# Kernel optimization log

Measured on AMD Instinct MI355X. Metric: run time of the kernel, lower is better.

Reference implementation:

```python
import jax, jax.numpy as jnp
import numpy as np

TEMP = 1.0  # temperature

def setup_inputs() -> dict:
    key = jax.random.key(0)
    ks = jax.random.split(key, 16)
    B, Cin, Cout, H, W, K, kk, A = 32, 64, 64, 128, 128, 4, 3, 16
    c_ = Cin + Cout
    r = lambda k, s: jax.random.normal(k, s, dtype=jnp.float32)
    return {
        'x': r(ks[0], (B, Cin, H, W)),
        'fc_w': r(ks[1], (A, Cin)) * 0.1,
        'ch_w': r(ks[2], (Cin, A)) * 0.1,
        'ch_b': jnp.zeros((Cin,), jnp.float32),
        'f_w': r(ks[3], (Cout, A)) * 0.1,
        'f_b': jnp.zeros((Cout,), jnp.float32),
        'sp_w': r(ks[4], (kk * kk, A)) * 0.1,
        'sp_b': jnp.zeros((kk * kk,), jnp.float32),
        'k_w': r(ks[5], (K, A)) * 0.1,
        'k_b': jnp.zeros((K,), jnp.float32),
        'fus_w1': r(ks[6], (c_ // 16, c_)) * 0.1,
        'fus_b1': jnp.zeros((c_ // 16,), jnp.float32),
        'fus_w2': r(ks[7], (c_, c_ // 16)) * 0.1,
        'fus_b2': jnp.zeros((c_,), jnp.float32),
        'weight': r(ks[8], (K, Cout, Cin, kk, kk)) * (1.0 / np.sqrt(Cin * kk * kk)),
    }

def reference(x, fc_w, ch_w, ch_b, f_w, f_b, sp_w, sp_b, k_w, k_b,
              fus_w1, fus_b1, fus_w2, fus_b2, weight):
    B, Cin, H, W = x.shape
    K, Cout, _, kk, _ = weight.shape
    # --- Attention branches (on globally pooled features) ---
    pooled = x.mean(axis=(2, 3))                      # (B, Cin)
    a = jax.nn.relu(pooled @ fc_w.T)                  # (B, A)
    ch_att = jax.nn.sigmoid(a @ ch_w.T + ch_b)        # (B, Cin)
    f_att = jax.nn.sigmoid(a @ f_w.T + f_b)           # (B, Cout)
    sp_att = jax.nn.sigmoid(a @ sp_w.T + sp_b).reshape(B, 1, 1, 1, kk, kk)
    k_att = jax.nn.softmax((a @ k_w.T + k_b) / TEMP, axis=1).reshape(B, K, 1, 1, 1, 1)
    # --- Attention fusion ---
    att = jnp.concatenate([ch_att, f_att], axis=1)    # (B, Cin+Cout)
    att2 = jax.nn.sigmoid(jax.nn.relu(att @ fus_w1.T + fus_b1) @ fus_w2.T + fus_b2)
    s1 = att2[:, :Cin].sum(axis=1)
    s2 = att2[:, Cin:].sum(axis=1)
    score = jax.nn.softmax(jnp.stack([s1, s2], axis=1) / TEMP, axis=1)
    w1 = score[:, 0][:, None, None, None]
    w2 = score[:, 1][:, None, None, None]
    # --- Apply channel attention, aggregate per-sample weights ---
    xm = w1 * x * ch_att[:, :, None, None]
    # (B,K,1,1,kk,kk)*(B,K,1,1,1,1)*(1,K,Cout,Cin,kk,kk) summed over K
    agg_w = (sp_att * k_att * weight[None]).sum(axis=1)  # (B, Cout, Cin, kk, kk)
    # --- Per-sample conv2d (stride 1, padding 1) ---
    def conv_one(xb, wb):
        return jax.lax.conv_general_dilated(
            xb[None], wb, window_strides=(1, 1), padding=[(1, 1), (1, 1)],
            dimension_numbers=('NCHW', 'OIHW', 'NCHW'))[0]
    out = jax.vmap(conv_one)(xm, agg_w)               # (B, Cout, H, W)
    return w2 * out * f_att[:, :, None, None]
```

## Files before the change

kernel.cpp:

```cpp
#include <hip/hip_runtime.h>
#include <math.h>
#include <stdint.h>

typedef short bf16x8 __attribute__((ext_vector_type(8)));
typedef float f32x16 __attribute__((ext_vector_type(16)));
typedef unsigned short ushort_t;

#define WP_PART 0
#define WP_CIN  65536
#define WP_COUT 67584
#define WP_SP9  69632
#define WP_K4   69920
#define WB_WFB  294912
#define WB_XB   2654208

static __device__ __forceinline__ unsigned f2bf(float f) {
  unsigned u = __builtin_bit_cast(unsigned, f);
  return (u + 0x7FFFu + ((u >> 16) & 1u)) >> 16;
}
static __device__ __forceinline__ unsigned pk2(float a, float b) {
  return f2bf(a) | (f2bf(b) << 16);
}

__global__ __launch_bounds__(256) void convert_kernel(const float* __restrict__ x,
                                                      ushort_t* __restrict__ xb,
                                                      float* __restrict__ part) {
  const int b    = blockIdx.x >> 5;
  const int band = blockIdx.x & 31;
  const int r0   = band << 2;
  const int t    = threadIdx.x;
  const int cp   = t & 31;
  const int seg  = t >> 5;

  __shared__ __align__(16) ushort_t tile[128 * 64];
  __shared__ float red[512];

  float sa = 0.f, sb = 0.f;
  const float* xa  = x + ((size_t)(b * 64 + 2 * cp) * 16384);
  const float* xb_ = xa + 16384;

  for (int r = 0; r < 4; ++r) {
    const int gr = r0 + r;
    const int p0 = gr * 128 + seg * 16;
    float4 a0 = *(const float4*)(xa + p0);
    float4 a1 = *(const float4*)(xa + p0 + 4);
    float4 a2 = *(const float4*)(xa + p0 + 8);
    float4 a3 = *(const float4*)(xa + p0 + 12);
    float4 b0 = *(const float4*)(xb_ + p0);
    float4 b1 = *(const float4*)(xb_ + p0 + 4);
    float4 b2 = *(const float4*)(xb_ + p0 + 8);
    float4 b3 = *(const float4*)(xb_ + p0 + 12);
    sa += (a0.x + a0.y + a0.z + a0.w) + (a1.x + a1.y + a1.z + a1.w) +
          (a2.x + a2.y + a2.z + a2.w) + (a3.x + a3.y + a3.z + a3.w);
    sb += (b0.x + b0.y + b0.z + b0.w) + (b1.x + b1.y + b1.z + b1.w) +
          (b2.x + b2.y + b2.z + b2.w) + (b3.x + b3.y + b3.z + b3.w);

    unsigned* tp = (unsigned*)tile;
    const int base = seg * 16 * 32 + cp;
    tp[base +  0 * 32] = pk2(a0.x, b0.x);
    tp[base +  1 * 32] = pk2(a0.y, b0.y);
    tp[base +  2 * 32] = pk2(a0.z, b0.z);
    tp[base +  3 * 32] = pk2(a0.w, b0.w);
    tp[base +  4 * 32] = pk2(a1.x, b1.x);
    tp[base +  5 * 32] = pk2(a1.y, b1.y);
    tp[base +  6 * 32] = pk2(a1.z, b1.z);
    tp[base +  7 * 32] = pk2(a1.w, b1.w);
    tp[base +  8 * 32] = pk2(a2.x, b2.x);
    tp[base +  9 * 32] = pk2(a2.y, b2.y);
    tp[base + 10 * 32] = pk2(a2.z, b2.z);
    tp[base + 11 * 32] = pk2(a2.w, b2.w);
    tp[base + 12 * 32] = pk2(a3.x, b3.x);
    tp[base + 13 * 32] = pk2(a3.y, b3.y);
    tp[base + 14 * 32] = pk2(a3.z, b3.z);
    tp[base + 15 * 32] = pk2(a3.w, b3.w);
    __syncthreads();

    ushort_t* xbr = xb + ((size_t)(b * 16384 + gr * 128)) * 64;
#pragma unroll
    for (int i = 0; i < 4; ++i) {
      const int s = i * 256 + t;
      uint4 v = *(const uint4*)((const char*)tile + s * 16);
      *(uint4*)(xbr + (size_t)s * 8) = v;
    }
    __syncthreads();
  }

  red[t] = sa;
  red[256 + t] = sb;
  __syncthreads();
  if (t < 64) {
    const int ci = t;
    const int base = (ci & 1) * 256 + (ci >> 1);
    float s = 0.f;
#pragma unroll
    for (int k = 0; k < 8; ++k) s += red[base + k * 32];
    part[((size_t)b * 32 + band) * 64 + ci] = s;
  }
}

__global__ __launch_bounds__(128) void att_kernel(
    const float* __restrict__ pin, int n_part,
    const float* __restrict__ fc_w, const float* __restrict__ ch_w, const float* __restrict__ ch_b,
    const float* __restrict__ f_w,  const float* __restrict__ f_b,
    const float* __restrict__ sp_w, const float* __restrict__ sp_b,
    const float* __restrict__ k_w,  const float* __restrict__ k_b,
    const float* __restrict__ fus_w1, const float* __restrict__ fus_b1,
    const float* __restrict__ fus_w2, const float* __restrict__ fus_b2,
    float* __restrict__ o_cin, float* __restrict__ o_cout,
    float* __restrict__ o_sp9, float* __restrict__ o_k4) {
  const int b = blockIdx.x;
  const int t = threadIdx.x;
  __shared__ float s_pool[64], s_a[16], s_att[128], s_sp[9], s_k[4], s_h[8],
      s_att2[128], s_red[2], s_w12[2];

  if (t < 64) {
    float s = 0.f;
    for (int g = 0; g < n_part; ++g) s += pin[((size_t)b * n_part + g) * 64 + t];
    s_pool[t] = s * (1.f / 16384.f);
  }
  __syncthreads();

  if (t < 16) {
    float s = 0.f;
    for (int c = 0; c < 64; ++c) s += s_pool[c] * fc_w[t * 64 + c];
    s_a[t] = fmaxf(s, 0.f);
  }
  __syncthreads();

  if (t < 64) {
    float s = ch_b[t];
    for (int j = 0; j < 16; ++j) s += s_a[j] * ch_w[t * 16 + j];
    s_att[t] = 1.f / (1.f + expf(-s));
  } else {
    const int o = t - 64;
    float s = f_b[o];
    for (int j = 0; j < 16; ++j) s += s_a[j] * f_w[o * 16 + j];
    s_att[t] = 1.f / (1.f + expf(-s));
  }
  if (t < 9) {
    float s = sp_b[t];
    for (int j = 0; j < 16; ++j) s += s_a[j] * sp_w[t * 16 + j];
    s_sp[t] = 1.f / (1.f + expf(-s));
  }
  if (t < 4) {
    float s = k_b[t];
    for (int j = 0; j < 16; ++j) s += s_a[j] * k_w[t * 16 + j];
    s_k[t] = s;
  }
  __syncthreads();

  if (t < 8) {
    float s = fus_b1[t];
    for (int c = 0; c < 128; ++c) s += s_att[c] * fus_w1[t * 128 + c];
    s_h[t] = fmaxf(s, 0.f);
  }
  if (t == 127) {
    float m = fmaxf(fmaxf(s_k[0], s_k[1]), fmaxf(s_k[2], s_k[3]));
    float e0 = expf(s_k[0] - m), e1 = expf(s_k[1] - m);
    float e2 = expf(s_k[2] - m), e3 = expf(s_k[3] - m);
    float inv = 1.f / (e0 + e1 + e2 + e3);
    s_k[0] = e0 * inv; s_k[1] = e1 * inv; s_k[2] = e2 * inv; s_k[3] = e3 * inv;
  }
  __syncthreads();

  {
    float s = fus_b2[t];
    for (int j = 0; j < 8; ++j) s += s_h[j] * fus_w2[t * 8 + j];
    s_att2[t] = 1.f / (1.f + expf(-s));
  }
  __syncthreads();

  if (t < 2) {
    float s = 0.f;
    for (int c = 0; c < 64; ++c) s += s_att2[t * 64 + c];
    s_red[t] = s;
  }
  __syncthreads();
  if (t == 0) {
    float m = fmaxf(s_red[0], s_red[1]);
    float e1 = expf(s_red[0] - m), e2 = expf(s_red[1] - m);
    float inv = 1.f / (e1 + e2);
    s_w12[0] = e1 * inv;
    s_w12[1] = e2 * inv;
  }
  __syncthreads();

  if (t < 64) {
    o_cin[b * 64 + t]  = s_w12[0] * s_att[t];
    o_cout[b * 64 + t] = s_w12[1] * s_att[64 + t];
  }
  if (t < 9) o_sp9[b * 9 + t] = s_sp[t];
  if (t < 4) o_k4[b * 4 + t] = s_k[t];
}

__global__ __launch_bounds__(256) void wf_kernel(const float* __restrict__ weight,
                                                 const float* __restrict__ cin,
                                                 const float* __restrict__ cout_,
                                                 const float* __restrict__ sp9,
                                                 const float* __restrict__ k4,
                                                 ushort_t* __restrict__ wfb) {
  const int bo = blockIdx.x;
  const int b = bo >> 6, o = bo & 63;
  const float co = cout_[b * 64 + o];
  const float k0 = k4[b * 4 + 0], k1 = k4[b * 4 + 1];
  const float k2 = k4[b * 4 + 2], k3 = k4[b * 4 + 3];
  for (int idx = threadIdx.x; idx < 576; idx += 256) {
    const int pq = idx >> 6, i = idx & 63;
    const size_t wi = ((size_t)o * 64 + i) * 9 + pq;
    float s = k0 * weight[wi] + k1 * weight[36864 + wi] +
              k2 * weight[73728 + wi] + k3 * weight[110592 + wi];
    float v = co * sp9[b * 9 + pq] * cin[b * 64 + i] * s;
    wfb[((size_t)(b * 9 + pq) * 64 + o) * 64 + i] = (ushort_t)f2bf(v);
  }
}

#define TILE_BYTES 25344
__global__ __launch_bounds__(512, 4) void conv_kernel(const ushort_t* __restrict__ xb,
                                                      const ushort_t* __restrict__ wfb,
                                                      float* __restrict__ out) {
  const int wg  = blockIdx.x;
  const int swz = (wg & 7) * 128 + (wg >> 3);
  const int b   = swz >> 5;
  const int h0  = (swz & 31) << 2;
  const int tid = threadIdx.x;
  const int lane = tid & 63;
  const int wid = tid >> 6;
  const int rw    = wid >> 1;
  const int nhalf = wid & 1;
  const int l31 = lane & 31;
  const int hi  = lane >> 5;

  __shared__ __align__(16) short sx[2 * 792 * 16];

  f32x16 acc00, acc01, acc10, acc11;
#pragma unroll
  for (int r = 0; r < 16; ++r) { acc00[r] = 0.f; acc01[r] = 0.f; acc10[r] = 0.f; acc11[r] = 0.f; }

  const ushort_t* wfb_b = wfb + (size_t)b * 36864;
  const ushort_t* xb_b  = xb + (size_t)b * 16384 * 64;

  int goff[4], loff[4];
  bool act[4], inb_[4];
#pragma unroll
  for (int i = 0; i < 4; ++i) {
    const int s = tid + i * 512;
    act[i] = s < 1560;
    const int s_ = act[i] ? s : 0;
    const int pl = s_ >> 1, oct = s_ & 1;
    const int r = pl / 130, tc = pl - r * 130;
    const int gr = h0 - 1 + r, gc = tc - 1;
    inb_[i] = act[i] && ((unsigned)gr < 128u) && ((unsigned)gc < 128u);
    goff[i] = (gr * 128 + gc) * 64 + oct * 8;
    const int px = r * 132 + tc;
    const int lg = px * 32 + oct * 16;
    loff[i] = lg ^ (((lg >> 7) & 7) << 4);
  }

  const uint4 zz = make_uint4(0u, 0u, 0u, 0u);
  uint4 st0, st1, st2, st3;

#define STAGE_LOAD(CH)                                                         \
  do {                                                                         \
    st0 = inb_[0] ? *(const uint4*)(xb_b + goff[0] + (CH) * 16) : zz;          \
    st1 = inb_[1] ? *(const uint4*)(xb_b + goff[1] + (CH) * 16) : zz;          \
    st2 = inb_[2] ? *(const uint4*)(xb_b + goff[2] + (CH) * 16) : zz;          \
    st3 = inb_[3] ? *(const uint4*)(xb_b + goff[3] + (CH) * 16) : zz;          \
  } while (0)

#define STAGE_WRITE(BUF)                                                       \
  do {                                                                         \
    *(uint4*)((char*)sx + (BUF) + loff[0]) = st0;                              \
    *(uint4*)((char*)sx + (BUF) + loff[1]) = st1;                              \
    *(uint4*)((char*)sx + (BUF) + loff[2]) = st2;                              \
    if (act[3]) *(uint4*)((char*)sx + (BUF) + loff[3]) = st3;                  \
  } while (0)

  STAGE_LOAD(0);
  STAGE_WRITE(0);
  __syncthreads();

#pragma unroll
  for (int ch = 0; ch < 4; ++ch) {
    if (ch < 3) STAGE_LOAD(ch + 1);
    const int bufb = (ch & 1) * TILE_BYTES;
    const int c0 = ch * 16;
#pragma unroll
    for (int p = 0; p < 3; ++p) {
#pragma unroll
      for (int q = 0; q < 3; ++q) {
        const int tap = p * 3 + q;
        bf16x8 af0 = *(const bf16x8*)(wfb_b + (tap * 64 + l31) * 64 + c0 + hi * 8);
        bf16x8 af1 = *(const bf16x8*)(wfb_b + (tap * 64 + 32 + l31) * 64 + c0 + hi * 8);
        const int pxa = (rw + p) * 132 + q + nhalf * 64 + l31;
        {
          const int lg = pxa * 32 + hi * 16;
          bf16x8 bf = *(const bf16x8*)((const char*)sx + bufb + (lg ^ (((lg >> 7) & 7) << 4)));
          acc00 = __builtin_amdgcn_mfma_f32_32x32x16_bf16(af0, bf, acc00, 0, 0, 0);
          acc10 = __builtin_amdgcn_mfma_f32_32x32x16_bf16(af1, bf, acc10, 0, 0, 0);
        }
        {
          const int lg = (pxa + 32) * 32 + hi * 16;
          bf16x8 bf = *(const bf16x8*)((const char*)sx + bufb + (lg ^ (((lg >> 7) & 7) << 4)));
          acc01 = __builtin_amdgcn_mfma_f32_32x32x16_bf16(af0, bf, acc01, 0, 0, 0);
          acc11 = __builtin_amdgcn_mfma_f32_32x32x16_bf16(af1, bf, acc11, 0, 0, 0);
        }
      }
    }
    if (ch < 3) {
      STAGE_WRITE(((ch + 1) & 1) * TILE_BYTES);
      __syncthreads();
    }
  }

  const int h = h0 + rw;
#define STORE_ACC(ACC, OFB, NT)                                                \
  do {                                                                         \
    const int col = nhalf * 64 + (NT) * 32 + l31;                              \
    _Pragma("unroll") for (int reg = 0; reg < 16; ++reg) {                     \
      const int o = (OFB) + (reg & 3) + ((reg >> 2) << 3) + (hi << 2);         \
      out[(((size_t)(b * 64 + o)) * 128 + h) * 128 + col] = (ACC)[reg];        \
    }                                                                          \
  } while (0)

  STORE_ACC(acc00, 0, 0);
  STORE_ACC(acc01, 0, 1);
  STORE_ACC(acc10, 32, 0);
  STORE_ACC(acc11, 32, 1);
#undef STORE_ACC
#undef STAGE_WRITE
#undef STAGE_LOAD
}

extern "C" void kernel_launch(void* const* d_in, const int* in_sizes, int n_in,
                              void* d_out, int out_size, void* d_ws, size_t ws_size,
                              hipStream_t stream) {
  const float* x      = (const float*)d_in[0];
  const float* fc_w   = (const float*)d_in[1];
  const float* ch_w   = (const float*)d_in[2];
  const float* ch_b   = (const float*)d_in[3];
  const float* f_w    = (const float*)d_in[4];
  const float* f_b    = (const float*)d_in[5];
  const float* sp_w   = (const float*)d_in[6];
  const float* sp_b   = (const float*)d_in[7];
  const float* k_w    = (const float*)d_in[8];
  const float* k_b    = (const float*)d_in[9];
  const float* fus_w1 = (const float*)d_in[10];
  const float* fus_b1 = (const float*)d_in[11];
  const float* fus_w2 = (const float*)d_in[12];
  const float* fus_b2 = (const float*)d_in[13];
  const float* weight = (const float*)d_in[14];
  float* ws  = (float*)d_ws;
  float* out = (float*)d_out;

  float* part  = ws + WP_PART;
  float* cin   = ws + WP_CIN;
  float* cout_ = ws + WP_COUT;
  float* sp9   = ws + WP_SP9;
  float* k4    = ws + WP_K4;
  ushort_t* wfb = (ushort_t*)((char*)d_ws + WB_WFB);
  ushort_t* xb  = (ushort_t*)((char*)d_ws + WB_XB);

  convert_kernel<<<1024, 256, 0, stream>>>(x, xb, part);
  att_kernel<<<32, 128, 0, stream>>>(part, 32, fc_w, ch_w, ch_b, f_w, f_b,
                                     sp_w, sp_b, k_w, k_b, fus_w1, fus_b1,
                                     fus_w2, fus_b2, cin, cout_, sp9, k4);
  wf_kernel<<<2048, 256, 0, stream>>>(weight, cin, cout_, sp9, k4, wfb);
  conv_kernel<<<1024, 512, 0, stream>>>(xb, wfb, out);
}
```

Baseline: 171.2 us.

## Halve conv output tile rows and split output channels across waves with prefetching

```diff
diff --git a/kernel.cpp b/kernel.cpp
--- a/kernel.cpp
+++ b/kernel.cpp
@@ -214,66 +214,91 @@
   }
 }
 
-#define TILE_BYTES 25344
+#define TILE_BYTES 16896
 __global__ __launch_bounds__(512, 4) void conv_kernel(const ushort_t* __restrict__ xb,
                                                       const ushort_t* __restrict__ wfb,
                                                       float* __restrict__ out) {
   const int wg  = blockIdx.x;
-  const int swz = (wg & 7) * 128 + (wg >> 3);
-  const int b   = swz >> 5;
-  const int h0  = (swz & 31) << 2;
+  const int swz = (wg & 7) * 256 + (wg >> 3);
+  const int b   = swz >> 6;
+  const int h0  = (swz & 63) << 1;
   const int tid = threadIdx.x;
   const int lane = tid & 63;
   const int wid = tid >> 6;
-  const int rw    = wid >> 1;
-  const int nhalf = wid & 1;
+  const int rw   = wid >> 2;
+  const int of32 = ((wid >> 1) & 1) << 5;
+  const int nh   = wid & 1;
   const int l31 = lane & 31;
   const int hi  = lane >> 5;
 
-  __shared__ __align__(16) short sx[2 * 792 * 16];
-
-  f32x16 acc00, acc01, acc10, acc11;
-#pragma unroll
-  for (int r = 0; r < 16; ++r) { acc00[r] = 0.f; acc01[r] = 0.f; acc10[r] = 0.f; acc11[r] = 0.f; }
+  __shared__ __align__(16) short sx[2 * 528 * 16];
+
+  f32x16 acc0, acc1;
+#pragma unroll
+  for (int r = 0; r < 16; ++r) { acc0[r] = 0.f; acc1[r] = 0.f; }
 
   const ushort_t* wfb_b = wfb + (size_t)b * 36864;
   const ushort_t* xb_b  = xb + (size_t)b * 16384 * 64;
 
-  int goff[4], loff[4];
-  bool act[4], inb_[4];
-#pragma unroll
-  for (int i = 0; i < 4; ++i) {
-    const int s = tid + i * 512;
-    act[i] = s < 1560;
-    const int s_ = act[i] ? s : 0;
-    const int pl = s_ >> 1, oct = s_ & 1;
+  int goff0, goff1, goff2, loff0, loff1, loff2;
+  bool inb0, inb1, inb2;
+  const bool act2 = tid < 16;
+  {
+    const int s = tid;
+    const int oct = s & 1, pl = s >> 1;
     const int r = pl / 130, tc = pl - r * 130;
     const int gr = h0 - 1 + r, gc = tc - 1;
-    inb_[i] = act[i] && ((unsigned)gr < 128u) && ((unsigned)gc < 128u);
-    goff[i] = (gr * 128 + gc) * 64 + oct * 8;
-    const int px = r * 132 + tc;
-    const int lg = px * 32 + oct * 16;
-    loff[i] = lg ^ (((lg >> 7) & 7) << 4);
+    inb0 = ((unsigned)gr < 128u) && ((unsigned)gc < 128u);
+    goff0 = (gr * 128 + gc) * 64 + oct * 8;
+    const int lg = (r * 132 + tc) * 32 + oct * 16;
+    loff0 = lg ^ ((((lg >> 7) & 7)) << 4);
+  }
+  {
+    const int s = tid + 512;
+    const int oct = s & 1, pl = s >> 1;
+    const int r = pl / 130, tc = pl - r * 130;
+    const int gr = h0 - 1 + r, gc = tc - 1;
+    inb1 = ((unsigned)gr < 128u) && ((unsigned)gc < 128u);
+    goff1 = (gr * 128 + gc) * 64 + oct * 8;
+    const int lg = (r * 132 + tc) * 32 + oct * 16;
+    loff1 = lg ^ ((((lg >> 7) & 7)) << 4);
+  }
+  {
+    const int s = act2 ? (tid + 1024) : 0;
+    const int oct = s & 1, pl = s >> 1;
+    const int r = pl / 130, tc = pl - r * 130;
+    const int gr = h0 - 1 + r, gc = tc - 1;
+    inb2 = act2 && ((unsigned)gr < 128u) && ((unsigned)gc < 128u);
+    goff2 = (gr * 128 + gc) * 64 + oct * 8;
+    const int lg = (r * 132 + tc) * 32 + oct * 16;
+    loff2 = lg ^ ((((lg >> 7) & 7)) << 4);
   }
 
   const uint4 zz = make_uint4(0u, 0u, 0u, 0u);
-  uint4 st0, st1, st2, st3;
-
-#define STAGE_LOAD(CH)                                                         \
-  do {                                                                         \
-    st0 = inb_[0] ? *(const uint4*)(xb_b + goff[0] + (CH) * 16) : zz;          \
-    st1 = inb_[1] ? *(const uint4*)(xb_b + goff[1] + (CH) * 16) : zz;          \
-    st2 = inb_[2] ? *(const uint4*)(xb_b + goff[2] + (CH) * 16) : zz;          \
-    st3 = inb_[3] ? *(const uint4*)(xb_b + goff[3] + (CH) * 16) : zz;          \
+  uint4 st0, st1, st2;
+
+#define STAGE_LOAD(CH)                                                   \
+  do {                                                                   \
+    st0 = inb0 ? *(const uint4*)(xb_b + goff0 + (CH) * 16) : zz;         \
+    st1 = inb1 ? *(const uint4*)(xb_b + goff1 + (CH) * 16) : zz;         \
+    st2 = inb2 ? *(const uint4*)(xb_b + goff2 + (CH) * 16) : zz;         \
   } while (0)
 
-#define STAGE_WRITE(BUF)                                                       \
-  do {                                                                         \
-    *(uint4*)((char*)sx + (BUF) + loff[0]) = st0;                              \
-    *(uint4*)((char*)sx + (BUF) + loff[1]) = st1;                              \
-    *(uint4*)((char*)sx + (BUF) + loff[2]) = st2;                              \
-    if (act[3]) *(uint4*)((char*)sx + (BUF) + loff[3]) = st3;                  \
+#define STAGE_WRITE(BUF)                                                 \
+  do {                                                                   \
+    *(uint4*)((char*)sx + (BUF) + loff0) = st0;                          \
+    *(uint4*)((char*)sx + (BUF) + loff1) = st1;                          \
+    if (act2) *(uint4*)((char*)sx + (BUF) + loff2) = st2;                \
   } while (0)
+
+  const int colbase = nh * 64 + l31;
+#define BX(BUFB, T, NT)                                                           \
+  (*(const bf16x8*)((const char*)sx + (BUFB) +                                    \
+    ((((rw + (T) / 3) * 132 + (T) % 3 + colbase + (NT) * 32) * 32 + hi * 16) ^    \
+     (((((rw + (T) / 3) * 132 + (T) % 3 + colbase + (NT) * 32) * 32 + hi * 16) >> 7) & 7) << 4)))
+
+#define AF(T, C0) \
+  (*(const bf16x8*)(wfb_b + ((T) * 64 + of32 + l31) * 64 + (C0) + hi * 8))
 
   STAGE_LOAD(0);
   STAGE_WRITE(0);
@@ -284,28 +309,23 @@
     if (ch < 3) STAGE_LOAD(ch + 1);
     const int bufb = (ch & 1) * TILE_BYTES;
     const int c0 = ch * 16;
-#pragma unroll
-    for (int p = 0; p < 3; ++p) {
-#pragma unroll
-      for (int q = 0; q < 3; ++q) {
-        const int tap = p * 3 + q;
-        bf16x8 af0 = *(const bf16x8*)(wfb_b + (tap * 64 + l31) * 64 + c0 + hi * 8);
-        bf16x8 af1 = *(const bf16x8*)(wfb_b + (tap * 64 + 32 + l31) * 64 + c0 + hi * 8);
-        const int pxa = (rw + p) * 132 + q + nhalf * 64 + l31;
-        {
-          const int lg = pxa * 32 + hi * 16;
-          bf16x8 bf = *(const bf16x8*)((const char*)sx + bufb + (lg ^ (((lg >> 7) & 7) << 4)));
-          acc00 = __builtin_amdgcn_mfma_f32_32x32x16_bf16(af0, bf, acc00, 0, 0, 0);
-          acc10 = __builtin_amdgcn_mfma_f32_32x32x16_bf16(af1, bf, acc10, 0, 0, 0);
-        }
-        {
-          const int lg = (pxa + 32) * 32 + hi * 16;
-          bf16x8 bf = *(const bf16x8*)((const char*)sx + bufb + (lg ^ (((lg >> 7) & 7) << 4)));
-          acc01 = __builtin_amdgcn_mfma_f32_32x32x16_bf16(af0, bf, acc01, 0, 0, 0);
-          acc11 = __builtin_amdgcn_mfma_f32_32x32x16_bf16(af1, bf, acc11, 0, 0, 0);
-        }
+
+    bf16x8 afA = AF(0, c0);
+    bf16x8 b0A = BX(bufb, 0, 0);
+    bf16x8 b1A = BX(bufb, 0, 1);
+#pragma unroll
+    for (int t = 0; t < 9; ++t) {
+      bf16x8 afB, b0B, b1B;
+      if (t < 8) {
+        afB = AF(t + 1, c0);
+        b0B = BX(bufb, t + 1, 0);
+        b1B = BX(bufb, t + 1, 1);
       }
+      acc0 = __builtin_amdgcn_mfma_f32_32x32x16_bf16(afA, b0A, acc0, 0, 0, 0);
+      acc1 = __builtin_amdgcn_mfma_f32_32x32x16_bf16(afA, b1A, acc1, 0, 0, 0);
+      if (t < 8) { afA = afB; b0A = b0B; b1A = b1B; }
     }
+
     if (ch < 3) {
       STAGE_WRITE(((ch + 1) & 1) * TILE_BYTES);
       __syncthreads();
@@ -313,20 +333,20 @@
   }
 
   const int h = h0 + rw;
-#define STORE_ACC(ACC, OFB, NT)                                                \
+#define STORE_ACC(ACC, NT)                                                     \
   do {                                                                         \
-    const int col = nhalf * 64 + (NT) * 32 + l31;                              \
+    const int col = nh * 64 + (NT) * 32 + l31;                                 \
     _Pragma("unroll") for (int reg = 0; reg < 16; ++reg) {                     \
-      const int o = (OFB) + (reg & 3) + ((reg >> 2) << 3) + (hi << 2);         \
+      const int o = of32 + (reg & 3) + ((reg >> 2) << 3) + (hi << 2);          \
       out[(((size_t)(b * 64 + o)) * 128 + h) * 128 + col] = (ACC)[reg];        \
     }                                                                          \
   } while (0)
 
-  STORE_ACC(acc00, 0, 0);
-  STORE_ACC(acc01, 0, 1);
-  STORE_ACC(acc10, 32, 0);
-  STORE_ACC(acc11, 32, 1);
+  STORE_ACC(acc0, 0);
+  STORE_ACC(acc1, 1);
 #undef STORE_ACC
+#undef AF
+#undef BX
 #undef STAGE_WRITE
 #undef STAGE_LOAD
 }
@@ -365,5 +385,5 @@
                                      sp_w, sp_b, k_w, k_b, fus_w1, fus_b1,
                                      fus_w2, fus_b2, cin, cout_, sp9, k4);
   wf_kernel<<<2048, 256, 0, stream>>>(weight, cin, cout_, sp9, k4, wfb);
-  conv_kernel<<<1024, 512, 0, stream>>>(xb, wfb, out);
-}
+  conv_kernel<<<2048, 512, 0, stream>>>(xb, wfb, out);
+}
```

New measurement: 168.6 us. About the same (-1.5%).
